# Performance work log

Hardware: AMD Instinct MI355X
Metric: run time of the kernel (lower is better)

## Reference

```python
import jax, jax.numpy as jnp
import numpy as np

H = 64      # hidden_size
IN = 3      # input_size (output_size + force dim)
OUT = 2     # output_size


def setup_inputs() -> dict:
    key = jax.random.key(0)
    ks = jax.random.split(key, 8)
    B, T, PL = 1024, 512, 300
    s = 1.0 / np.sqrt(H)  # pytorch default init range
    x = jax.random.normal(ks[0], (B, T, IN), jnp.float32)
    force = jax.random.normal(ks[1], (B, PL - 1, 1), jnp.float32)
    W_ih = jax.random.uniform(ks[2], (4 * H, IN), jnp.float32, -s, s)
    W_hh = jax.random.uniform(ks[3], (4 * H, H), jnp.float32, -s, s)
    b_ih = jax.random.uniform(ks[4], (4 * H,), jnp.float32, -s, s)
    b_hh = jax.random.uniform(ks[5], (4 * H,), jnp.float32, -s, s)
    W_out = jax.random.uniform(ks[6], (OUT, H), jnp.float32, -s, s)
    b_out = jax.random.uniform(ks[7], (OUT,), jnp.float32, -s, s)
    return {"x": x, "force": force, "W_ih": W_ih, "W_hh": W_hh,
            "b_ih": b_ih, "b_hh": b_hh, "W_out": W_out, "b_out": b_out,
            "predict_length": PL}


def _lstm_cell(h, c, x_t, W_ih, W_hh, b):
    # pytorch gate order: i, f, g, o
    g = x_t @ W_ih.T + h @ W_hh.T + b
    i, f, gg, o = jnp.split(g, 4, axis=-1)
    c_new = jax.nn.sigmoid(f) * c + jax.nn.sigmoid(i) * jnp.tanh(gg)
    h_new = jax.nn.sigmoid(o) * jnp.tanh(c_new)
    return h_new, c_new


def reference(x, force, W_ih, W_hh, b_ih, b_hh, W_out, b_out, predict_length):
    b = b_ih + b_hh
    B = x.shape[0]
    h0 = jnp.zeros((B, H), x.dtype)
    c0 = jnp.zeros((B, H), x.dtype)

    # ---- encoder: run LSTM over full input sequence ----
    def enc_step(carry, x_t):
        h, c = carry
        h, c = _lstm_cell(h, c, x_t, W_ih, W_hh, b)
        return (h, c), h
    (h, c), _ = jax.lax.scan(enc_step, (h0, c0), jnp.swapaxes(x, 0, 1))

    # first decoder output = out(last encoder hidden)
    y0 = h @ W_out.T + b_out  # [B, OUT]

    def dec_step(carry, f_t):
        h, c, y = carry
        x_t = jnp.concatenate([y, f_t], axis=-1)  # [B, OUT+1] == [B, IN]
        h, c = _lstm_cell(h, c, x_t, W_ih, W_hh, b)
        y = h @ W_out.T + b_out
        return (h, c, y), y
    f_seq = jnp.swapaxes(force, 0, 1)[: predict_length - 1]  # [PL-1, B, 1]
    _, ys = jax.lax.scan(dec_step, (h, c, y0), f_seq)  # [PL-1, B, OUT]

    out = jnp.concatenate([y0[:, None, :], jnp.swapaxes(ys, 0, 1)], axis=1)
    return out  # [B, predict_length, OUT]
```

## Files before the change

kernel.cpp:

```cpp
#include <hip/hip_runtime.h>

#define Hh 64
#define INPUT 3
#define OUTD 2
#define BATCH 1024
#define BT 4
#define TENC 512
#define PLEN 300
#define GSTR 260
#define HSTR 120

#define LOG2E 1.44269504088896340736f

typedef short  short8 __attribute__((ext_vector_type(8)));
typedef float  f32x4  __attribute__((ext_vector_type(4)));

__device__ __forceinline__ float sigm_(float x) {
    float t = __builtin_amdgcn_exp2f(-x * LOG2E);
    return __builtin_amdgcn_rcpf(1.0f + t);
}
__device__ __forceinline__ float tanh_(float x) {
    float t = __builtin_amdgcn_exp2f(x * (2.0f * LOG2E));
    return fmaf(-2.0f, __builtin_amdgcn_rcpf(1.0f + t), 1.0f);
}
__device__ __forceinline__ void bf16split(float v, unsigned short& hi, unsigned short& lo) {
    unsigned int b = __float_as_uint(v);
    hi = (unsigned short)(b >> 16);
    float r = v - __uint_as_float((unsigned int)hi << 16);
    lo = (unsigned short)(__float_as_uint(r) >> 16);
}

__global__ __launch_bounds__(256, 1)
void lstm_forecast_kernel(const float* __restrict__ x,
                          const float* __restrict__ force,
                          const float* __restrict__ W_ih,
                          const float* __restrict__ W_hh,
                          const float* __restrict__ b_ih,
                          const float* __restrict__ b_hh,
                          const float* __restrict__ W_out,
                          const float* __restrict__ b_out,
                          float* __restrict__ out)
{
    const int tid  = threadIdx.x;
    const int lane = tid & 63;
    const int wv   = tid >> 6;
    const int m    = lane & 15;
    const int kg   = (lane >> 4) * 8;
    const int b0   = blockIdx.x * BT;

    __shared__ __align__(16) float          x_s[BT][TENC * INPUT];
    __shared__ __align__(16) float          f_s[BT][PLEN - 1];
    __shared__ __align__(16) float          G_s[BT][GSTR];
    __shared__ __align__(16) unsigned short h_hiT[BT][HSTR];
    __shared__ __align__(16) unsigned short h_loT[BT][HSTR];

    {
        const float4* xg = reinterpret_cast<const float4*>(x + (size_t)b0 * TENC * INPUT);
        float4* xs = reinterpret_cast<float4*>(&x_s[0][0]);
        for (int i = tid; i < BT * TENC * INPUT / 4; i += 256) xs[i] = xg[i];
        const float* fg = force + (size_t)b0 * (PLEN - 1);
        float* fs = &f_s[0][0];
        for (int i = tid; i < BT * (PLEN - 1); i += 256) fs[i] = fg[i];
        unsigned short* hh = &h_hiT[0][0];
        unsigned short* hl = &h_loT[0][0];
        for (int i = tid; i < BT * HSTR; i += 256) { hh[i] = 0; hl[i] = 0; }
    }
    __syncthreads();
    if (tid < BT) h_hiT[tid][64 + 3] = 0x3F80;
    if (tid < BT * 4 && (tid & 3) < 3) {
        const int bb = tid >> 2, j = tid & 3;
        unsigned short xh, xl; bf16split(x_s[bb][j], xh, xl);
        h_hiT[bb][64 + j] = xh; h_loT[bb][64 + j] = xl;
    }

    short8 Ahi[4][3], Alo[4][3];
    #pragma unroll
    for (int i = 0; i < 4; ++i) {
        const int row = 64 * wv + 16 * i + m;
        #pragma unroll
        for (int ks = 0; ks < 2; ++ks) {
            const float* wp = W_hh + (size_t)row * Hh + ks * 32 + kg;
            short8 h8 = {0,0,0,0,0,0,0,0}, l8 = {0,0,0,0,0,0,0,0};
            #pragma unroll
            for (int j = 0; j < 8; ++j) {
                unsigned short h_, l_; bf16split(wp[j], h_, l_);
                h8[j] = (short)h_; l8[j] = (short)l_;
            }
            Ahi[i][ks] = h8; Alo[i][ks] = l8;
        }
        {
            short8 h8 = {0,0,0,0,0,0,0,0}, l8 = {0,0,0,0,0,0,0,0};
            if (kg == 0) {
                float v0 = W_ih[row * INPUT + 0], v1 = W_ih[row * INPUT + 1];
                float v2 = W_ih[row * INPUT + 2], v3 = b_ih[row] + b_hh[row];
                unsigned short h_, l_;
                bf16split(v0, h_, l_); h8[0] = h_; l8[0] = l_;
                bf16split(v1, h_, l_); h8[1] = h_; l8[1] = l_;
                bf16split(v2, h_, l_); h8[2] = h_; l8[2] = l_;
                bf16split(v3, h_, l_); h8[3] = h_; l8[3] = l_;
            }
            Ahi[i][2] = h8; Alo[i][2] = l8;
        }
    }

    const float wo0 = W_out[lane];
    const float wo1 = W_out[Hh + lane];
    const float bo0 = b_out[0], bo1 = b_out[1];
    float* outb = out + (size_t)(b0 + wv) * (PLEN * OUTD);

    float c = 0.0f;
    __syncthreads();

    auto phase1 = [&]() {
        const int bcl = lane & 3;
        short8 bh[3], bl[3];
        #pragma unroll
        for (int ks = 0; ks < 3; ++ks) {
            bh[ks] = *reinterpret_cast<const short8*>(&h_hiT[bcl][ks * 32 + kg]);
            bl[ks] = *reinterpret_cast<const short8*>(&h_loT[bcl][ks * 32 + kg]);
        }
        #pragma unroll
        for (int i = 0; i < 4; ++i) {
            f32x4 acc = {0.0f, 0.0f, 0.0f, 0.0f};
            #pragma unroll
            for (int ks = 0; ks < 3; ++ks) {
                acc = __builtin_amdgcn_mfma_f32_16x16x32_bf16(Ahi[i][ks], bh[ks], acc, 0, 0, 0);
                acc = __builtin_amdgcn_mfma_f32_16x16x32_bf16(Alo[i][ks], bh[ks], acc, 0, 0, 0);
                acc = __builtin_amdgcn_mfma_f32_16x16x32_bf16(Ahi[i][ks], bl[ks], acc, 0, 0, 0);
            }
            if (m < BT) {
                *reinterpret_cast<f32x4*>(&G_s[m][64 * wv + 16 * i + (lane >> 4) * 4]) = acc;
            }
        }
    };

    auto phase2 = [&](bool do_y, int dpos, int fidx, bool enc_next, int tnext) {
        const float gi = G_s[wv][lane];
        const float gf = G_s[wv][64 + lane];
        const float gg = G_s[wv][128 + lane];
        const float go = G_s[wv][192 + lane];
        const float si = sigm_(gi);
        const float sf = sigm_(gf);
        const float sg = tanh_(gg);
        const float so = sigm_(go);
        c = fmaf(sf, c, si * sg);
        const float h = so * tanh_(c);
        unsigned short hh, hl; bf16split(h, hh, hl);
        h_hiT[wv][lane] = hh;
        h_loT[wv][lane] = hl;
        if (enc_next && lane < 3) {
            unsigned short xh, xl; bf16split(x_s[wv][tnext * INPUT + lane], xh, xl);
            h_hiT[wv][64 + lane] = xh; h_loT[wv][64 + lane] = xl;
        }
        if (do_y) {
            float p0 = wo0 * h, p1 = wo1 * h;
            #pragma unroll
            for (int msk = 1; msk < 64; msk <<= 1) {
                p0 += __shfl_xor(p0, msk, 64);
                p1 += __shfl_xor(p1, msk, 64);
            }
            const float y0 = p0 + bo0, y1 = p1 + bo1;
            if (lane == 0) *reinterpret_cast<float2*>(outb + dpos * OUTD) = make_float2(y0, y1);
            if (lane < 3) {
                const float v = (lane == 0) ? y0 : (lane == 1) ? y1 : f_s[wv][fidx];
                unsigned short xh, xl; bf16split(v, xh, xl);
                h_hiT[wv][64 + lane] = xh; h_loT[wv][64 + lane] = xl;
            }
        }
    };

    for (int t = 0; t < TENC; ++t) {
        phase1();
        __syncthreads();
        if (t < TENC - 1) phase2(false, 0, 0, true, t + 1);
        else              phase2(true, 0, 0, false, 0);
        __syncthreads();
    }
    for (int s = 0; s < PLEN - 1; ++s) {
        phase1();
        __syncthreads();
        const int fnext = (s + 1 <= PLEN - 2) ? (s + 1) : (PLEN - 2);
        phase2(true, s + 1, fnext, false, 0);
        __syncthreads();
    }
}

extern "C" void kernel_launch(void* const* d_in, const int* in_sizes, int n_in,
                              void* d_out, int out_size, void* d_ws, size_t ws_size,
                              hipStream_t stream) {
    const float* x     = (const float*)d_in[0];
    const float* force = (const float*)d_in[1];
    const float* W_ih  = (const float*)d_in[2];
    const float* W_hh  = (const float*)d_in[3];
    const float* b_ih  = (const float*)d_in[4];
    const float* b_hh  = (const float*)d_in[5];
    const float* W_out = (const float*)d_in[6];
    const float* b_out = (const float*)d_in[7];
    float* out = (float*)d_out;

    lstm_forecast_kernel<<<BATCH / BT, 256, 0, stream>>>(
        x, force, W_ih, W_hh, b_ih, b_hh, W_out, b_out, out);
}
```

Before: 657.2 us.

## Fold output projection into decoder weights and split LSTM work across 8 waves

Removes the separate input-feature MFMA k-slice by adding the x·W_ih and bias terms in fp32 on the gate path. For the decoder, W_ih·W_out is folded into W_hh and the biases, so the feedback y no longer has to be reduced before the next step's matmul. Blocks now run 8 waves (512 threads, 2 blocks per CU): each wave computes 32 gate rows. Pairs of waves redundantly evaluate the cell, one storing h and the other emitting y off the critical path. This cuts MFMA count per wave and the shuffle-reduction latency on the recurrence, at the cost of redundant gate math and changed rounding from the folded weights.

```diff
diff --git a/kernel.cpp b/kernel.cpp
--- a/kernel.cpp
+++ b/kernel.cpp
@@ -4,11 +4,11 @@
 #define INPUT 3
 #define OUTD 2
 #define BATCH 1024
-#define BT 4
+#define NBB 4
 #define TENC 512
 #define PLEN 300
-#define GSTR 260
-#define HSTR 120
+#define GP 260
+#define HP 80
 
 #define LOG2E 1.44269504088896340736f
 
@@ -16,12 +16,10 @@
 typedef float  f32x4  __attribute__((ext_vector_type(4)));
 
 __device__ __forceinline__ float sigm_(float x) {
-    float t = __builtin_amdgcn_exp2f(-x * LOG2E);
-    return __builtin_amdgcn_rcpf(1.0f + t);
+    return __builtin_amdgcn_rcpf(1.0f + __builtin_amdgcn_exp2f(-x * LOG2E));
 }
 __device__ __forceinline__ float tanh_(float x) {
-    float t = __builtin_amdgcn_exp2f(x * (2.0f * LOG2E));
-    return fmaf(-2.0f, __builtin_amdgcn_rcpf(1.0f + t), 1.0f);
+    return fmaf(-2.0f, __builtin_amdgcn_rcpf(1.0f + __builtin_amdgcn_exp2f(x * (2.0f * LOG2E))), 1.0f);
 }
 __device__ __forceinline__ void bf16split(float v, unsigned short& hi, unsigned short& lo) {
     unsigned int b = __float_as_uint(v);
@@ -30,7 +28,9 @@
     lo = (unsigned short)(__float_as_uint(r) >> 16);
 }
 
-__global__ __launch_bounds__(256, 1)
+#define MFMA16(A, B, C) __builtin_amdgcn_mfma_f32_16x16x32_bf16((A), (B), (C), 0, 0, 0)
+
+__global__ __launch_bounds__(512, 2)
 void lstm_forecast_kernel(const float* __restrict__ x,
                           const float* __restrict__ force,
                           const float* __restrict__ W_ih,
@@ -45,142 +45,158 @@
     const int lane = tid & 63;
     const int wv   = tid >> 6;
     const int m    = lane & 15;
-    const int kg   = (lane >> 4) * 8;
-    const int b0   = blockIdx.x * BT;
-
-    __shared__ __align__(16) float          x_s[BT][TENC * INPUT];
-    __shared__ __align__(16) float          f_s[BT][PLEN - 1];
-    __shared__ __align__(16) float          G_s[BT][GSTR];
-    __shared__ __align__(16) unsigned short h_hiT[BT][HSTR];
-    __shared__ __align__(16) unsigned short h_loT[BT][HSTR];
-
-    {
-        const float4* xg = reinterpret_cast<const float4*>(x + (size_t)b0 * TENC * INPUT);
-        float4* xs = reinterpret_cast<float4*>(&x_s[0][0]);
-        for (int i = tid; i < BT * TENC * INPUT / 4; i += 256) xs[i] = xg[i];
-        const float* fg = force + (size_t)b0 * (PLEN - 1);
-        float* fs = &f_s[0][0];
-        for (int i = tid; i < BT * (PLEN - 1); i += 256) fs[i] = fg[i];
-        unsigned short* hh = &h_hiT[0][0];
-        unsigned short* hl = &h_loT[0][0];
-        for (int i = tid; i < BT * HSTR; i += 256) { hh[i] = 0; hl[i] = 0; }
-    }
+    const int g4   = lane >> 4;
+    const int kg   = g4 * 8;
+    const int bb   = wv >> 1;
+    const int odd  = wv & 1;
+    const int u    = lane;
+    const int b0   = blockIdx.x * NBB;
+
+    __shared__ __align__(16) float          x_s[NBB][TENC * 4];
+    __shared__ __align__(16) float          f_s[NBB][PLEN - 1];
+    __shared__ __align__(16) float          G_s[NBB][GP];
+    __shared__ __align__(16) unsigned short h_hi[NBB * HP];
+    __shared__ __align__(16) unsigned short h_lo[NBB * HP];
+
+    for (int i = tid; i < NBB * TENC * INPUT; i += 512) {
+        const int b_  = i / (TENC * INPUT);
+        const int rem = i - b_ * (TENC * INPUT);
+        const int t   = rem / 3;
+        const int c_  = rem - 3 * t;
+        x_s[b_][t * 4 + c_] = x[(size_t)(b0 + b_) * (TENC * INPUT) + rem];
+    }
+    for (int i = tid; i < NBB * (PLEN - 1); i += 512) {
+        const int b_ = i / (PLEN - 1);
+        const int d_ = i - b_ * (PLEN - 1);
+        f_s[b_][d_] = force[(size_t)(b0 + b_) * (PLEN - 1) + d_];
+    }
+    if (tid < NBB * HP) { h_hi[tid] = 0; h_lo[tid] = 0; }
+
+    float wie[4][3], be[4], wd[4], bd[4];
+    const float bo0 = b_out[0], bo1 = b_out[1];
+    #pragma unroll
+    for (int g_ = 0; g_ < 4; ++g_) {
+        const int r = g_ * 64 + u;
+        wie[g_][0] = W_ih[r * 3 + 0];
+        wie[g_][1] = W_ih[r * 3 + 1];
+        wie[g_][2] = W_ih[r * 3 + 2];
+        be[g_] = b_ih[r] + b_hh[r];
+        wd[g_] = wie[g_][2];
+        bd[g_] = be[g_] + wie[g_][0] * bo0 + wie[g_][1] * bo1;
+    }
+    const float wo0 = W_out[u];
+    const float wo1 = W_out[64 + u];
+
+    short8 AH[2][2], AL[2][2];
+    auto build_frags = [&](bool aug) {
+        #pragma unroll
+        for (int TT = 0; TT < 2; ++TT) {
+            const int r = (2 * wv + TT) * 16 + m;
+            const float wr0 = W_ih[r * 3 + 0];
+            const float wr1 = W_ih[r * 3 + 1];
+            #pragma unroll
+            for (int ks = 0; ks < 2; ++ks) {
+                const float* wp = W_hh + (size_t)r * Hh + ks * 32 + kg;
+                const float* q0 = W_out + ks * 32 + kg;
+                const float* q1 = W_out + 64 + ks * 32 + kg;
+                short8 h8, l8;
+                #pragma unroll
+                for (int j = 0; j < 8; ++j) {
+                    float w = wp[j];
+                    if (aug) w = fmaf(wr0, q0[j], fmaf(wr1, q1[j], w));
+                    unsigned short hh_, ll_;
+                    bf16split(w, hh_, ll_);
+                    h8[j] = (short)hh_; l8[j] = (short)ll_;
+                }
+                AH[TT][ks] = h8; AL[TT][ks] = l8;
+            }
+        }
+    };
+    build_frags(false);
+
+    float c = 0.0f;
+
+    auto phase1 = [&]() {
+        const int sb = (m & 3) * HP;
+        const short8 bh0 = *reinterpret_cast<const short8*>(&h_hi[sb + kg]);
+        const short8 bh1 = *reinterpret_cast<const short8*>(&h_hi[sb + 32 + kg]);
+        const short8 bl0 = *reinterpret_cast<const short8*>(&h_lo[sb + kg]);
+        const short8 bl1 = *reinterpret_cast<const short8*>(&h_lo[sb + 32 + kg]);
+        #pragma unroll
+        for (int TT = 0; TT < 2; ++TT) {
+            f32x4 acc = {0.0f, 0.0f, 0.0f, 0.0f};
+            acc = MFMA16(AH[TT][0], bh0, acc);
+            acc = MFMA16(AL[TT][0], bh0, acc);
+            acc = MFMA16(AH[TT][0], bl0, acc);
+            acc = MFMA16(AH[TT][1], bh1, acc);
+            acc = MFMA16(AL[TT][1], bh1, acc);
+            acc = MFMA16(AH[TT][1], bl1, acc);
+            if (m < 4) {
+                *reinterpret_cast<f32x4*>(&G_s[m][(2 * wv + TT) * 16 + 4 * g4]) = acc;
+            }
+        }
+    };
+
+    auto gates = [&](float pi, float pf, float pg, float po) -> float {
+        const float si = sigm_(pi);
+        const float sf = sigm_(pf);
+        const float sg = tanh_(pg);
+        const float so = sigm_(po);
+        c = fmaf(sf, c, si * sg);
+        return so * tanh_(c);
+    };
+    auto store_h = [&](float h) {
+        unsigned short hh_, hl_;
+        bf16split(h, hh_, hl_);
+        h_hi[bb * HP + u] = hh_;
+        h_lo[bb * HP + u] = hl_;
+    };
+    auto emit_y = [&](float h, int pos) {
+        float p0 = wo0 * h, p1 = wo1 * h;
+        #pragma unroll
+        for (int msk = 1; msk < 64; msk <<= 1) {
+            p0 += __shfl_xor(p0, msk, 64);
+            p1 += __shfl_xor(p1, msk, 64);
+        }
+        if (lane == 0) {
+            *reinterpret_cast<float2*>(out + (size_t)(b0 + bb) * (PLEN * OUTD) + pos * OUTD)
+                = make_float2(p0 + bo0, p1 + bo1);
+        }
+    };
+
     __syncthreads();
-    if (tid < BT) h_hiT[tid][64 + 3] = 0x3F80;
-    if (tid < BT * 4 && (tid & 3) < 3) {
-        const int bb = tid >> 2, j = tid & 3;
-        unsigned short xh, xl; bf16split(x_s[bb][j], xh, xl);
-        h_hiT[bb][64 + j] = xh; h_loT[bb][64 + j] = xl;
-    }
-
-    short8 Ahi[4][3], Alo[4][3];
-    #pragma unroll
-    for (int i = 0; i < 4; ++i) {
-        const int row = 64 * wv + 16 * i + m;
-        #pragma unroll
-        for (int ks = 0; ks < 2; ++ks) {
-            const float* wp = W_hh + (size_t)row * Hh + ks * 32 + kg;
-            short8 h8 = {0,0,0,0,0,0,0,0}, l8 = {0,0,0,0,0,0,0,0};
-            #pragma unroll
-            for (int j = 0; j < 8; ++j) {
-                unsigned short h_, l_; bf16split(wp[j], h_, l_);
-                h8[j] = (short)h_; l8[j] = (short)l_;
-            }
-            Ahi[i][ks] = h8; Alo[i][ks] = l8;
-        }
-        {
-            short8 h8 = {0,0,0,0,0,0,0,0}, l8 = {0,0,0,0,0,0,0,0};
-            if (kg == 0) {
-                float v0 = W_ih[row * INPUT + 0], v1 = W_ih[row * INPUT + 1];
-                float v2 = W_ih[row * INPUT + 2], v3 = b_ih[row] + b_hh[row];
-                unsigned short h_, l_;
-                bf16split(v0, h_, l_); h8[0] = h_; l8[0] = l_;
-                bf16split(v1, h_, l_); h8[1] = h_; l8[1] = l_;
-                bf16split(v2, h_, l_); h8[2] = h_; l8[2] = l_;
-                bf16split(v3, h_, l_); h8[3] = h_; l8[3] = l_;
-            }
-            Ahi[i][2] = h8; Alo[i][2] = l8;
-        }
-    }
-
-    const float wo0 = W_out[lane];
-    const float wo1 = W_out[Hh + lane];
-    const float bo0 = b_out[0], bo1 = b_out[1];
-    float* outb = out + (size_t)(b0 + wv) * (PLEN * OUTD);
-
-    float c = 0.0f;
-    __syncthreads();
-
-    auto phase1 = [&]() {
-        const int bcl = lane & 3;
-        short8 bh[3], bl[3];
-        #pragma unroll
-        for (int ks = 0; ks < 3; ++ks) {
-            bh[ks] = *reinterpret_cast<const short8*>(&h_hiT[bcl][ks * 32 + kg]);
-            bl[ks] = *reinterpret_cast<const short8*>(&h_loT[bcl][ks * 32 + kg]);
-        }
-        #pragma unroll
-        for (int i = 0; i < 4; ++i) {
-            f32x4 acc = {0.0f, 0.0f, 0.0f, 0.0f};
-            #pragma unroll
-            for (int ks = 0; ks < 3; ++ks) {
-                acc = __builtin_amdgcn_mfma_f32_16x16x32_bf16(Ahi[i][ks], bh[ks], acc, 0, 0, 0);
-                acc = __builtin_amdgcn_mfma_f32_16x16x32_bf16(Alo[i][ks], bh[ks], acc, 0, 0, 0);
-                acc = __builtin_amdgcn_mfma_f32_16x16x32_bf16(Ahi[i][ks], bl[ks], acc, 0, 0, 0);
-            }
-            if (m < BT) {
-                *reinterpret_cast<f32x4*>(&G_s[m][64 * wv + 16 * i + (lane >> 4) * 4]) = acc;
-            }
-        }
-    };
-
-    auto phase2 = [&](bool do_y, int dpos, int fidx, bool enc_next, int tnext) {
-        const float gi = G_s[wv][lane];
-        const float gf = G_s[wv][64 + lane];
-        const float gg = G_s[wv][128 + lane];
-        const float go = G_s[wv][192 + lane];
-        const float si = sigm_(gi);
-        const float sf = sigm_(gf);
-        const float sg = tanh_(gg);
-        const float so = sigm_(go);
-        c = fmaf(sf, c, si * sg);
-        const float h = so * tanh_(c);
-        unsigned short hh, hl; bf16split(h, hh, hl);
-        h_hiT[wv][lane] = hh;
-        h_loT[wv][lane] = hl;
-        if (enc_next && lane < 3) {
-            unsigned short xh, xl; bf16split(x_s[wv][tnext * INPUT + lane], xh, xl);
-            h_hiT[wv][64 + lane] = xh; h_loT[wv][64 + lane] = xl;
-        }
-        if (do_y) {
-            float p0 = wo0 * h, p1 = wo1 * h;
-            #pragma unroll
-            for (int msk = 1; msk < 64; msk <<= 1) {
-                p0 += __shfl_xor(p0, msk, 64);
-                p1 += __shfl_xor(p1, msk, 64);
-            }
-            const float y0 = p0 + bo0, y1 = p1 + bo1;
-            if (lane == 0) *reinterpret_cast<float2*>(outb + dpos * OUTD) = make_float2(y0, y1);
-            if (lane < 3) {
-                const float v = (lane == 0) ? y0 : (lane == 1) ? y1 : f_s[wv][fidx];
-                unsigned short xh, xl; bf16split(v, xh, xl);
-                h_hiT[wv][64 + lane] = xh; h_loT[wv][64 + lane] = xl;
-            }
-        }
-    };
 
     for (int t = 0; t < TENC; ++t) {
         phase1();
         __syncthreads();
-        if (t < TENC - 1) phase2(false, 0, 0, true, t + 1);
-        else              phase2(true, 0, 0, false, 0);
-        __syncthreads();
-    }
+        const float4 xq = *reinterpret_cast<const float4*>(&x_s[bb][t * 4]);
+        float pi = G_s[bb][u]       + be[0];
+        float pf = G_s[bb][64 + u]  + be[1];
+        float pg = G_s[bb][128 + u] + be[2];
+        float po = G_s[bb][192 + u] + be[3];
+        pi = fmaf(wie[0][0], xq.x, pi); pi = fmaf(wie[0][1], xq.y, pi); pi = fmaf(wie[0][2], xq.z, pi);
+        pf = fmaf(wie[1][0], xq.x, pf); pf = fmaf(wie[1][1], xq.y, pf); pf = fmaf(wie[1][2], xq.z, pf);
+        pg = fmaf(wie[2][0], xq.x, pg); pg = fmaf(wie[2][1], xq.y, pg); pg = fmaf(wie[2][2], xq.z, pg);
+        po = fmaf(wie[3][0], xq.x, po); po = fmaf(wie[3][1], xq.y, po); po = fmaf(wie[3][2], xq.z, po);
+        const float h = gates(pi, pf, pg, po);
+        if (!odd)                store_h(h);
+        else if (t == TENC - 1)  emit_y(h, 0);
+        __syncthreads();
+    }
+
+    build_frags(true);
+
     for (int s = 0; s < PLEN - 1; ++s) {
         phase1();
         __syncthreads();
-        const int fnext = (s + 1 <= PLEN - 2) ? (s + 1) : (PLEN - 2);
-        phase2(true, s + 1, fnext, false, 0);
+        const float fv = f_s[bb][s];
+        float pi = G_s[bb][u]       + fmaf(wd[0], fv, bd[0]);
+        float pf = G_s[bb][64 + u]  + fmaf(wd[1], fv, bd[1]);
+        float pg = G_s[bb][128 + u] + fmaf(wd[2], fv, bd[2]);
+        float po = G_s[bb][192 + u] + fmaf(wd[3], fv, bd[3]);
+        const float h = gates(pi, pf, pg, po);
+        if (!odd) store_h(h);
+        else      emit_y(h, s + 1);
         __syncthreads();
     }
 }
@@ -198,6 +214,6 @@
     const float* b_out = (const float*)d_in[7];
     float* out = (float*)d_out;
 
-    lstm_forecast_kernel<<<BATCH / BT, 256, 0, stream>>>(
+    lstm_forecast_kernel<<<BATCH / NBB, 512, 0, stream>>>(
         x, force, W_ih, W_hh, b_ih, b_hh, W_out, b_out, out);
 }
```

After: 616.6 us. 1.07x faster.
